# Kernel optimization log

Measured on AMD Instinct MI355X. Metric: run time of the kernel, lower is better.

## Reference

```python
import jax, jax.numpy as jnp
import numpy as np

B, C, H, W = 4, 128, 128, 128
K = 9          # 3x3 kernel taps
TAU, BETA = 0.5, 10.0


def conv3x3(x, w, b):
    # x: (B,Cin,H,W), w: (Cout,Cin,3,3), stride 1, padding 1
    y = jax.lax.conv_general_dilated(
        x, w, window_strides=(1, 1), padding=((1, 1), (1, 1)),
        dimension_numbers=('NCHW', 'OIHW', 'NCHW'))
    return y + b[None, :, None, None]


def bilinear_sample(x, py, px):
    # x: (B,C,H,W); py,px: (B,K,H,W) fractional coords -> (B,C,K,H,W), zero outside
    Hi, Wi = x.shape[2], x.shape[3]
    y0 = jnp.floor(py); x0 = jnp.floor(px)
    y1 = y0 + 1.0;      x1 = x0 + 1.0
    ly = py - y0; lx = px - x0
    hy = 1.0 - ly; hx = 1.0 - lx
    xf = x.reshape(x.shape[0], x.shape[1], -1)  # (B,C,HW)

    def corner(yc, xc, wgt):
        valid = (yc >= 0) & (yc <= Hi - 1) & (xc >= 0) & (xc <= Wi - 1)
        yi = jnp.clip(yc, 0, Hi - 1).astype(jnp.int32)
        xi = jnp.clip(xc, 0, Wi - 1).astype(jnp.int32)
        idx = (yi * Wi + xi).reshape(yc.shape[0], -1)  # (B, K*H*W)
        g = jax.vmap(lambda f, i: f[:, i])(xf, idx)    # (B,C,K*H*W)
        g = g.reshape(x.shape[0], x.shape[1], *yc.shape[1:])  # (B,C,K,H,W)
        return g * (wgt * valid.astype(wgt.dtype))[:, None]

    return (corner(y0, x0, hy * hx) + corner(y0, x1, hy * lx)
            + corner(y1, x0, ly * hx) + corner(y1, x1, ly * lx))


def modulated_dcn(x, offset, mask, w, b):
    # offset: (B,2K,H,W) layout (dy,dx) per tap; mask: (B,K,H,W)
    Bn, Cn, Hn, Wn = x.shape
    off = offset.reshape(Bn, K, 2, Hn, Wn)
    dy, dx = off[:, :, 0], off[:, :, 1]
    ky, kx = jnp.meshgrid(jnp.arange(3), jnp.arange(3), indexing='ij')
    base_y = (ky.reshape(-1) - 1).astype(x.dtype)  # dilation=1, padding=1, stride=1
    base_x = (kx.reshape(-1) - 1).astype(x.dtype)
    hh = jnp.arange(Hn, dtype=x.dtype)
    ww = jnp.arange(Wn, dtype=x.dtype)
    py = hh[None, None, :, None] + base_y[None, :, None, None] + dy  # (B,K,H,W)
    px = ww[None, None, None, :] + base_x[None, :, None, None] + dx
    samp = bilinear_sample(x, py, px) * mask[:, None]  # (B,C,K,H,W)
    out = jnp.einsum('bckhw,ock->bohw', samp, w.reshape(w.shape[0], w.shape[1], K))
    return out + b[None, :, None, None]


def setup_inputs() -> dict:
    key = jax.random.key(0)
    ks = jax.random.split(key, 8)
    x = jax.random.normal(ks[0], (B, C, H, W), dtype=jnp.float32)
    U = jax.random.uniform(ks[1], (B, 1, H, W), dtype=jnp.float32)
    # conv_offset_mask: (3*K, C+1, 3, 3); small scale -> offsets of O(1) pixel
    w_om = jax.random.normal(ks[2], (3 * K, C + 1, 3, 3), dtype=jnp.float32) * 0.01
    b_om = jnp.zeros((3 * K,), dtype=jnp.float32)
    kaiming = float(np.sqrt(2.0 / (C * 9)))
    w_dcn = jax.random.normal(ks[3], (C, C, 3, 3), dtype=jnp.float32) * kaiming
    b_dcn = jnp.zeros((C,), dtype=jnp.float32)
    w1 = jax.random.normal(ks[4], (C, C, 3, 3), dtype=jnp.float32) * kaiming
    b1 = jnp.zeros((C,), dtype=jnp.float32)
    w2 = jax.random.normal(ks[5], (C, C, 3, 3), dtype=jnp.float32) * float(np.sqrt(1.0 / (C * 9)))
    b2 = jnp.zeros((C,), dtype=jnp.float32)
    return {"x": x, "U": U, "w_om": w_om, "b_om": b_om, "w_dcn": w_dcn,
            "b_dcn": b_dcn, "w1": w1, "b1": b1, "w2": w2, "b2": b2}


def reference(x, U, w_om, b_om, w_dcn, b_dcn, w1, b1, w2, b2):
    U = jnp.clip(U, 0.0, 1.0)
    guide = jnp.concatenate([x, U], axis=1)                # (B,C+1,H,W)
    om = conv3x3(guide, w_om, b_om)                        # (B,3K,H,W)
    offset = om[:, :2 * K]
    mask = 2.0 * jax.nn.sigmoid(om[:, 2 * K:])
    z = modulated_dcn(x, offset, mask, w_dcn, b_dcn)
    r = jax.nn.relu(conv3x3(z, w1, b1))
    r = conv3x3(r, w2, b2)
    gate = jax.nn.sigmoid(BETA * (U - TAU))
    return jax.nn.relu(x + r * gate)
```

## Files before the change

kernel.cpp:

```cpp
#include <hip/hip_runtime.h>
#include <math.h>

typedef unsigned int uint;
typedef unsigned short ushort;
typedef __attribute__((ext_vector_type(8))) __bf16 bf16x8;
typedef __attribute__((ext_vector_type(2))) __bf16 bf16x2;
typedef __attribute__((ext_vector_type(4))) float f32x4;
typedef __attribute__((ext_vector_type(2))) float f32x2;

#define HW 16384

__device__ __forceinline__ ushort f2bf(float f) {
    uint u = __float_as_uint(f);
    u += 0x7fffu + ((u >> 16) & 1u);
    return (ushort)(u >> 16);
}
__device__ __forceinline__ void bhmap(int& b, int& h) {
    int lin = blockIdx.y * (int)gridDim.x + blockIdx.x;
    int n = (lin & 7) * 64 + (lin >> 3);
    h = n & 127;
    b = n >> 7;
}
__device__ __forceinline__ int swz(int row, int chunk) {
    return row * 128 + ((chunk ^ (row & 15)) << 3);
}
__device__ __forceinline__ void gl2lds16(const ushort* g, ushort* l) {
    __builtin_amdgcn_global_load_lds(
        (const __attribute__((address_space(1))) uint*)g,
        (__attribute__((address_space(3))) uint*)l,
        16, 0, 0);
}
__device__ __forceinline__ uint blend2(uint a, uint b, uint c, uint d,
                                       float w00, float w01, float w10, float w11) {
    f32x2 va = { __uint_as_float(a << 16), __uint_as_float(a & 0xffff0000u) };
    f32x2 vb = { __uint_as_float(b << 16), __uint_as_float(b & 0xffff0000u) };
    f32x2 vc = { __uint_as_float(c << 16), __uint_as_float(c & 0xffff0000u) };
    f32x2 vd = { __uint_as_float(d << 16), __uint_as_float(d & 0xffff0000u) };
    f32x2 v = va * w00 + vb * w01 + vc * w10 + vd * w11;
    bf16x2 pk; pk[0] = (__bf16)v[0]; pk[1] = (__bf16)v[1];
    uint r; __builtin_memcpy(&r, &pk, 4);
    return r;
}

__global__ __launch_bounds__(256) void prep_w(
    const float* __restrict__ wd, const float* __restrict__ w1,
    const float* __restrict__ w2, const float* __restrict__ wom,
    ushort* __restrict__ wdt, ushort* __restrict__ w1t,
    ushort* __restrict__ w2t, ushort* __restrict__ womt,
    float* __restrict__ womu)
{
    int i = blockIdx.x * 256 + threadIdx.x;
    if (i < 147456) {
        int k = i >> 14, oc = (i >> 7) & 127, d = i & 127;
        int ci = (((d >> 3) ^ (oc & 15)) << 3) | (d & 7);
        int s = (oc * 128 + ci) * 9 + k;
        wdt[i] = f2bf(wd[s]);
        w1t[i] = f2bf(w1[s]);
        w2t[i] = f2bf(w2[s]);
    }
    if (i < 36864) {
        int k = i >> 12, oc = (i >> 7) & 31, d = i & 127;
        int ci = (((d >> 3) ^ (oc & 15)) << 3) | (d & 7);
        womt[i] = (oc < 27) ? f2bf(wom[(oc * 129 + ci) * 9 + k]) : (ushort)0;
    }
    if (i < 288) {
        int k = i >> 5, oc = i & 31;
        womu[i] = (oc < 27) ? wom[(oc * 129 + 128) * 9 + k] : 0.f;
    }
}

__global__ __launch_bounds__(256) void prep_xt(
    const float* __restrict__ x, ushort* __restrict__ xt)
{
    int b, h; bhmap(b, h);
    const int tid = threadIdx.x;
    __shared__ __align__(16) ushort T[128 * 136];
    const int w0 = tid & 127, cg = tid >> 7;
#pragma unroll 4
    for (int it = 0; it < 64; it++) {
        int c = it * 2 + cg;
        float f = x[((size_t)(b * 128 + c)) * HW + h * 128 + w0];
        T[w0 * 136 + c] = f2bf(f);
    }
    __syncthreads();
    const int w1 = tid >> 1, half = tid & 1;
    uint4* dst = (uint4*)(xt + (((size_t)b * HW) + h * 128 + w1) * 128 + half * 64);
    const uint4* src = (const uint4*)&T[w1 * 136 + half * 64];
#pragma unroll
    for (int c8 = 0; c8 < 8; c8++) dst[c8] = src[c8];
}

__global__ __launch_bounds__(512, 4) void k_om(
    const ushort* __restrict__ xt, const float* __restrict__ U,
    const ushort* __restrict__ womt, const float* __restrict__ womu,
    const float* __restrict__ bom, float* __restrict__ omt)
{
    int b, h; bhmap(b, h);
    const int tid = threadIdx.x;
    const int wid = tid >> 6, lane = tid & 63, lq = lane & 15, quad = lane >> 4;
    const int pixbase = wid * 16;

    __shared__ __align__(16) ushort As[130 * 128];
    __shared__ __align__(16) ushort Bs[3][32 * 128];
    __shared__ float U3[3 * 130];
    __shared__ float wu[288];

    f32x4 acc[2];
#pragma unroll
    for (int j = 0; j < 2; j++)
#pragma unroll
        for (int r = 0; r < 4; r++) acc[j][r] = 0.f;

    for (int s = tid; s < 390; s += 512) {
        int r = s / 130, c = s % 130, gy = h - 1 + r, gx = c - 1;
        float v = 0.f;
        if ((unsigned)gy < 128u && (unsigned)gx < 128u) {
            v = U[(size_t)b * HW + gy * 128 + gx];
            v = fminf(fmaxf(v, 0.f), 1.f);
        }
        U3[s] = v;
    }
    if (tid < 288) wu[tid] = womu[tid];

    const size_t xb = (size_t)b * HW * 128;
#pragma unroll
    for (int dyi = 0; dyi < 3; dyi++) {
        int gy = h + dyi - 1;
        for (int c = tid; c < 2080; c += 512) {
            int r = c >> 4, ch = c & 15, gx = r - 1;
            uint4 v = {0, 0, 0, 0};
            if ((unsigned)gy < 128u && (unsigned)gx < 128u)
                v = *(const uint4*)(xt + xb + ((size_t)gy * 128 + gx) * 128 + ch * 8);
            *(uint4*)&As[swz(r, ch)] = v;
        }
#pragma unroll
        for (int t = 0; t < 3; t++)
            gl2lds16(womt + (dyi * 3 + t) * 4096 + tid * 8, &Bs[t][wid * 512]);
        __syncthreads();
#pragma unroll
        for (int dx = 0; dx < 3; dx++) {
#pragma unroll
            for (int kk = 0; kk < 4; kk++) {
                int chunk = kk * 4 + quad;
                bf16x8 av = *(const bf16x8*)&As[swz(pixbase + lq + dx, chunk)];
                bf16x8 bv[2];
#pragma unroll
                for (int j = 0; j < 2; j++) bv[j] = *(const bf16x8*)&Bs[dx][swz(j * 16 + lq, chunk)];
#pragma unroll
                for (int j = 0; j < 2; j++)
                    acc[j] = __builtin_amdgcn_mfma_f32_16x16x32_bf16(av, bv[j], acc[j], 0, 0, 0);
            }
        }
        __syncthreads();
    }

#pragma unroll
    for (int j = 0; j < 2; j++) {
        int oc = j * 16 + lq;
        if (oc < 27) {
            float bias = bom[oc];
#pragma unroll
            for (int r = 0; r < 4; r++) {
                int pix = pixbase + quad * 4 + r;
                float v = acc[j][r] + bias;
#pragma unroll
                for (int t = 0; t < 9; t++)
                    v += U3[(t / 3) * 130 + pix + (t % 3)] * wu[t * 32 + oc];
                if (oc >= 18) v = 2.f / (1.f + __expf(-v));
                omt[((size_t)b * HW + h * 128 + pix) * 32 + oc] = v;
            }
        }
    }
}

__global__ __launch_bounds__(512, 4) void k_dcn(
    const ushort* __restrict__ xt, const float* __restrict__ omt,
    const ushort* __restrict__ wdt, const float* __restrict__ bdcn,
    ushort* __restrict__ zt)
{
    int b, h; bhmap(b, h);
    const int tid = threadIdx.x;
    const int wid = tid >> 6, lane = tid & 63, lq = lane & 15, quad = lane >> 4;
    const int pixbase = (wid & 1) * 64, ocbase = (wid >> 1) * 32;

    __shared__ __align__(16) ushort As[128 * 128];
    __shared__ __align__(16) ushort Bs[128 * 128];
    __shared__ __align__(16) int tbl[2][128][8];

    const int sc = lane & 15;
    const int sp = lane >> 4;

    f32x4 acc[4][2];
#pragma unroll
    for (int i = 0; i < 4; i++)
#pragma unroll
        for (int j = 0; j < 2; j++)
#pragma unroll
            for (int r = 0; r < 4; r++) acc[i][j][r] = 0.f;

    const float* omrow = omt + ((size_t)b * HW + h * 128) * 32;
    const ushort* xtb = xt + (size_t)b * HW * 128;

    auto build = [&](int k, int buf) {
        if (tid < 128) {
            int p = tid;
            float dyv = omrow[p * 32 + 2 * k];
            float dxv = omrow[p * 32 + 2 * k + 1];
            float m   = omrow[p * 32 + 18 + k];
            float fy = (float)(h + k / 3 - 1) + dyv;
            float fx = (float)(p + k % 3 - 1) + dxv;
            float y0f = floorf(fy), x0f = floorf(fx);
            float ly = fy - y0f, lx = fx - x0f;
            float hy = 1.f - ly, hx = 1.f - lx;
            bool vy0 = (y0f >= 0.f) && (y0f <= 127.f);
            bool vy1 = (y0f >= -1.f) && (y0f <= 126.f);
            bool vx0 = (x0f >= 0.f) && (x0f <= 127.f);
            bool vx1 = (x0f >= -1.f) && (x0f <= 126.f);
            float w00 = (vy0 && vx0) ? hy * hx * m : 0.f;
            float w01 = (vy0 && vx1) ? hy * lx * m : 0.f;
            float w10 = (vy1 && vx0) ? ly * hx * m : 0.f;
            float w11 = (vy1 && vx1) ? ly * lx * m : 0.f;
            int iy0 = min(max((int)y0f, 0), 127);
            int iy1 = min(max((int)y0f + 1, 0), 127);
            int ix0 = min(max((int)x0f, 0), 127);
            int ix1 = min(max((int)x0f + 1, 0), 127);
            int* tp = &tbl[buf][p][0];
            tp[0] = (iy0 * 128 + ix0) * 128;
            tp[1] = (iy0 * 128 + ix1) * 128;
            tp[2] = (iy1 * 128 + ix0) * 128;
            tp[3] = (iy1 * 128 + ix1) * 128;
            ((float*)tp)[4] = w00; ((float*)tp)[5] = w01;
            ((float*)tp)[6] = w10; ((float*)tp)[7] = w11;
        }
    };

    build(0, 0);
    __syncthreads();

    for (int k = 0; k < 9; k++) {
        const int buf = k & 1;
        {
            const ushort* wsrc = wdt + (size_t)k * 16384;
#pragma unroll
            for (int c = 0; c < 4; c++)
                gl2lds16(wsrc + c * 4096 + tid * 8, &Bs[c * 4096 + wid * 512]);
        }
        const ushort* basep = xtb + sc * 8;
#pragma unroll 2
        for (int r = 0; r < 4; r++) {
            int p = r * 32 + wid * 4 + sp;
            int4 off = *(const int4*)&tbl[buf][p][0];
            f32x4 wv = *(const f32x4*)((const float*)&tbl[buf][p][0] + 4);
            uint4 q00 = *(const uint4*)(basep + off.x);
            uint4 q01 = *(const uint4*)(basep + off.y);
            uint4 q10 = *(const uint4*)(basep + off.z);
            uint4 q11 = *(const uint4*)(basep + off.w);
            uint4 st;
            st.x = blend2(q00.x, q01.x, q10.x, q11.x, wv[0], wv[1], wv[2], wv[3]);
            st.y = blend2(q00.y, q01.y, q10.y, q11.y, wv[0], wv[1], wv[2], wv[3]);
            st.z = blend2(q00.z, q01.z, q10.z, q11.z, wv[0], wv[1], wv[2], wv[3]);
            st.w = blend2(q00.w, q01.w, q10.w, q11.w, wv[0], wv[1], wv[2], wv[3]);
            *(uint4*)&As[swz(p, sc)] = st;
        }
        __syncthreads();
        if (k < 8) build(k + 1, buf ^ 1);
#pragma unroll
        for (int kk = 0; kk < 4; kk++) {
            int chunk = kk * 4 + quad;
            bf16x8 av[4], bv[2];
#pragma unroll
            for (int i = 0; i < 4; i++) av[i] = *(const bf16x8*)&As[swz(pixbase + i * 16 + lq, chunk)];
#pragma unroll
            for (int j = 0; j < 2; j++) bv[j] = *(const bf16x8*)&Bs[swz(ocbase + j * 16 + lq, chunk)];
#pragma unroll
            for (int i = 0; i < 4; i++)
#pragma unroll
                for (int j = 0; j < 2; j++)
                    acc[i][j] = __builtin_amdgcn_mfma_f32_16x16x32_bf16(av[i], bv[j], acc[i][j], 0, 0, 0);
        }
        __syncthreads();
    }

    size_t prow = ((size_t)b * HW + h * 128) * 128;
#pragma unroll
    for (int j = 0; j < 2; j++) {
        int oc = ocbase + j * 16 + lq;
        float bias = bdcn[oc];
#pragma unroll
        for (int i = 0; i < 4; i++)
#pragma unroll
            for (int r = 0; r < 4; r++) {
                int pix = pixbase + i * 16 + quad * 4 + r;
                zt[prow + (size_t)pix * 128 + oc] = f2bf(acc[i][j][r] + bias);
            }
    }
}

__global__ __launch_bounds__(512, 4) void k_conv1(
    const ushort* __restrict__ zt, const ushort* __restrict__ w1t,
    const float* __restrict__ b1, ushort* __restrict__ r1t)
{
    int b, h; bhmap(b, h);
    const int tid = threadIdx.x;
    const int wid = tid >> 6, lane = tid & 63, lq = lane & 15, quad = lane >> 4;
    const int pixbase = (wid & 1) * 64, ocbase = (wid >> 1) * 32;

    __shared__ __align__(16) ushort As[130 * 128];
    __shared__ __align__(16) ushort Bs[128 * 128];

    f32x4 acc[4][2];
#pragma unroll
    for (int i = 0; i < 4; i++)
#pragma unroll
        for (int j = 0; j < 2; j++)
#pragma unroll
            for (int r = 0; r < 4; r++) acc[i][j][r] = 0.f;

    const size_t zb = (size_t)b * HW * 128;
    for (int t9 = 0; t9 < 9; t9++) {
        const int dyi = t9 / 3, dx = t9 % 3;
        if (dx == 0) {
            int gy = h + dyi - 1;
            for (int c = tid; c < 2080; c += 512) {
                int r = c >> 4, ch = c & 15, gx = r - 1;
                uint4 v = {0, 0, 0, 0};
                if ((unsigned)gy < 128u && (unsigned)gx < 128u)
                    v = *(const uint4*)(zt + zb + ((size_t)gy * 128 + gx) * 128 + ch * 8);
                *(uint4*)&As[swz(r, ch)] = v;
            }
        }
        {
            const ushort* wsrc = w1t + (size_t)t9 * 16384;
#pragma unroll
            for (int c = 0; c < 4; c++)
                gl2lds16(wsrc + c * 4096 + tid * 8, &Bs[c * 4096 + wid * 512]);
        }
        __syncthreads();
#pragma unroll
        for (int kk = 0; kk < 4; kk++) {
            int chunk = kk * 4 + quad;
            bf16x8 av[4], bv[2];
#pragma unroll
            for (int i = 0; i < 4; i++)
                av[i] = *(const bf16x8*)&As[swz(pixbase + i * 16 + lq + dx, chunk)];
#pragma unroll
            for (int j = 0; j < 2; j++) bv[j] = *(const bf16x8*)&Bs[swz(ocbase + j * 16 + lq, chunk)];
#pragma unroll
            for (int i = 0; i < 4; i++)
#pragma unroll
                for (int j = 0; j < 2; j++)
                    acc[i][j] = __builtin_amdgcn_mfma_f32_16x16x32_bf16(av[i], bv[j], acc[i][j], 0, 0, 0);
        }
        __syncthreads();
    }

    size_t prow = ((size_t)b * HW + h * 128) * 128;
#pragma unroll
    for (int j = 0; j < 2; j++) {
        int oc = ocbase + j * 16 + lq;
        float bias = b1[oc];
#pragma unroll
        for (int i = 0; i < 4; i++)
#pragma unroll
            for (int r = 0; r < 4; r++) {
                int pix = pixbase + i * 16 + quad * 4 + r;
                r1t[prow + (size_t)pix * 128 + oc] = f2bf(fmaxf(acc[i][j][r] + bias, 0.f));
            }
    }
}

__global__ __launch_bounds__(512, 4) void k_conv2(
    const ushort* __restrict__ r1t, const ushort* __restrict__ w2t,
    const float* __restrict__ b2, const float* __restrict__ x,
    const float* __restrict__ U, float* __restrict__ out)
{
    int b, h; bhmap(b, h);
    const int tid = threadIdx.x;
    const int wid = tid >> 6, lane = tid & 63, lq = lane & 15, quad = lane >> 4;
    const int mbase = (wid & 1) * 64;
    const int nbase = (wid >> 1) * 32;

    __shared__ __align__(16) ushort As[128 * 128];
    __shared__ __align__(16) ushort Bs[130 * 128];

    f32x4 acc[4][2];
#pragma unroll
    for (int i = 0; i < 4; i++)
#pragma unroll
        for (int j = 0; j < 2; j++)
#pragma unroll
            for (int r = 0; r < 4; r++) acc[i][j][r] = 0.f;

    const size_t rb = (size_t)b * HW * 128;
    for (int t9 = 0; t9 < 9; t9++) {
        const int dyi = t9 / 3, dx = t9 % 3;
        if (dx == 0) {
            int gy = h + dyi - 1;
            for (int c = tid; c < 2080; c += 512) {
                int r = c >> 4, ch = c & 15, gx = r - 1;
                uint4 v = {0, 0, 0, 0};
                if ((unsigned)gy < 128u && (unsigned)gx < 128u)
                    v = *(const uint4*)(r1t + rb + ((size_t)gy * 128 + gx) * 128 + ch * 8);
                *(uint4*)&Bs[swz(r, ch)] = v;
            }
        }
        {
            const ushort* wsrc = w2t + (size_t)t9 * 16384;
#pragma unroll
            for (int c = 0; c < 4; c++)
                gl2lds16(wsrc + c * 4096 + tid * 8, &As[c * 4096 + wid * 512]);
        }
        __syncthreads();
#pragma unroll
        for (int kk = 0; kk < 4; kk++) {
            int chunk = kk * 4 + quad;
            bf16x8 av[4], bv[2];
#pragma unroll
            for (int i = 0; i < 4; i++) av[i] = *(const bf16x8*)&As[swz(mbase + i * 16 + lq, chunk)];
#pragma unroll
            for (int j = 0; j < 2; j++)
                bv[j] = *(const bf16x8*)&Bs[swz(nbase + j * 16 + lq + dx, chunk)];
#pragma unroll
            for (int i = 0; i < 4; i++)
#pragma unroll
                for (int j = 0; j < 2; j++)
                    acc[i][j] = __builtin_amdgcn_mfma_f32_16x16x32_bf16(av[i], bv[j], acc[i][j], 0, 0, 0);
        }
        __syncthreads();
    }

#pragma unroll
    for (int j = 0; j < 2; j++) {
        int pix = nbase + j * 16 + lq;
        float u = U[(size_t)b * HW + h * 128 + pix];
        u = fminf(fmaxf(u, 0.f), 1.f);
        float g = 1.f / (1.f + __expf(-10.f * (u - 0.5f)));
#pragma unroll
        for (int i = 0; i < 4; i++) {
            f32x4 b4 = *(const f32x4*)&b2[mbase + i * 16 + quad * 4];
#pragma unroll
            for (int r = 0; r < 4; r++) {
                int oc = mbase + i * 16 + quad * 4 + r;
                size_t idx = ((size_t)(b * 128 + oc)) * HW + h * 128 + pix;
                float v = acc[i][j][r] + b4[r];
                out[idx] = fmaxf(x[idx] + v * g, 0.f);
            }
        }
    }
}

extern "C" void kernel_launch(void* const* d_in, const int* in_sizes, int n_in,
                              void* d_out, int out_size, void* d_ws, size_t ws_size,
                              hipStream_t stream)
{
    const float* x     = (const float*)d_in[0];
    const float* U     = (const float*)d_in[1];
    const float* w_om  = (const float*)d_in[2];
    const float* b_om  = (const float*)d_in[3];
    const float* w_dcn = (const float*)d_in[4];
    const float* b_dcn = (const float*)d_in[5];
    const float* w1    = (const float*)d_in[6];
    const float* b1    = (const float*)d_in[7];
    const float* w2    = (const float*)d_in[8];
    const float* b2    = (const float*)d_in[9];
    float* out = (float*)d_out;

    char* p = (char*)d_ws;
    ushort* xt   = (ushort*)p; p += (size_t)4 * HW * 128 * 2;
    ushort* zt   = (ushort*)p; p += (size_t)4 * HW * 128 * 2;
    ushort* r1t  = (ushort*)p; p += (size_t)4 * HW * 128 * 2;
    float*  omt  = (float*)p;  p += (size_t)4 * HW * 32 * 4;
    ushort* wdt  = (ushort*)p; p += 147456 * 2;
    ushort* w1t  = (ushort*)p; p += 147456 * 2;
    ushort* w2t  = (ushort*)p; p += 147456 * 2;
    ushort* womt = (ushort*)p; p += 36864 * 2;
    float*  womu = (float*)p;  p += 288 * 4;

    prep_w<<<576, 256, 0, stream>>>(w_dcn, w1, w2, w_om, wdt, w1t, w2t, womt, womu);
    prep_xt<<<dim3(128, 4), 256, 0, stream>>>(x, xt);
    k_om<<<dim3(128, 4), 512, 0, stream>>>(xt, U, womt, womu, b_om, omt);
    k_dcn<<<dim3(128, 4), 512, 0, stream>>>(xt, omt, wdt, b_dcn, zt);
    k_conv1<<<dim3(128, 4), 512, 0, stream>>>(zt, w1t, b1, r1t);
    k_conv2<<<dim3(128, 4), 512, 0, stream>>>(r1t, w2t, b2, x, U, out);
}
```

Baseline: 216.0 us.

## Process two output rows per block in conv1/conv2 to share weight tiles

Each conv block now covers two image rows with 1024 threads instead of one row with 512, so every per-tap 128x128 weight tile loaded into LDS feeds twice as many MFMAs. This halves weight traffic from global memory and the LDS fill work per output row. The cost is a larger LDS footprint (about 98 KB for the two input-row tiles plus the weight tile) and half as many blocks (256), which limits occupancy and how many blocks run concurrently per CU.

```diff
diff --git a/kernel.cpp b/kernel.cpp
--- a/kernel.cpp
+++ b/kernel.cpp
@@ -20,6 +20,12 @@
     int n = (lin & 7) * 64 + (lin >> 3);
     h = n & 127;
     b = n >> 7;
+}
+__device__ __forceinline__ void bhmap2r(int& b, int& h0) {
+    int lin = blockIdx.y * (int)gridDim.x + blockIdx.x;
+    int n = (lin & 7) * 32 + (lin >> 3);
+    h0 = (n & 63) * 2;
+    b = n >> 6;
 }
 __device__ __forceinline__ int swz(int row, int chunk) {
     return row * 128 + ((chunk ^ (row & 15)) << 3);
@@ -296,16 +302,19 @@
     }
 }
 
-__global__ __launch_bounds__(512, 4) void k_conv1(
+__global__ __launch_bounds__(1024, 4) void k_conv1(
     const ushort* __restrict__ zt, const ushort* __restrict__ w1t,
     const float* __restrict__ b1, ushort* __restrict__ r1t)
 {
-    int b, h; bhmap(b, h);
+    int b, h0; bhmap2r(b, h0);
     const int tid = threadIdx.x;
     const int wid = tid >> 6, lane = tid & 63, lq = lane & 15, quad = lane >> 4;
-    const int pixbase = (wid & 1) * 64, ocbase = (wid >> 1) * 32;
-
-    __shared__ __align__(16) ushort As[130 * 128];
+    const int row = wid >> 3;
+    const int pixbase = (wid & 1) * 64;
+    const int ocbase = ((wid >> 1) & 3) * 32;
+    const int rowoff = row * 16640;
+
+    __shared__ __align__(16) ushort As[2 * 130 * 128];
     __shared__ __align__(16) ushort Bs[128 * 128];
 
     f32x4 acc[4][2];
@@ -320,20 +329,23 @@
     for (int t9 = 0; t9 < 9; t9++) {
         const int dyi = t9 / 3, dx = t9 % 3;
         if (dx == 0) {
-            int gy = h + dyi - 1;
-            for (int c = tid; c < 2080; c += 512) {
-                int r = c >> 4, ch = c & 15, gx = r - 1;
-                uint4 v = {0, 0, 0, 0};
-                if ((unsigned)gy < 128u && (unsigned)gx < 128u)
-                    v = *(const uint4*)(zt + zb + ((size_t)gy * 128 + gx) * 128 + ch * 8);
-                *(uint4*)&As[swz(r, ch)] = v;
+#pragma unroll
+            for (int rr = 0; rr < 2; rr++) {
+                int gy = h0 + rr + dyi - 1;
+                for (int c = tid; c < 2080; c += 1024) {
+                    int r = c >> 4, ch = c & 15, gx = r - 1;
+                    uint4 v = {0, 0, 0, 0};
+                    if ((unsigned)gy < 128u && (unsigned)gx < 128u)
+                        v = *(const uint4*)(zt + zb + ((size_t)gy * 128 + gx) * 128 + ch * 8);
+                    *(uint4*)&As[rr * 16640 + swz(r, ch)] = v;
+                }
             }
         }
         {
             const ushort* wsrc = w1t + (size_t)t9 * 16384;
 #pragma unroll
-            for (int c = 0; c < 4; c++)
-                gl2lds16(wsrc + c * 4096 + tid * 8, &Bs[c * 4096 + wid * 512]);
+            for (int c = 0; c < 2; c++)
+                gl2lds16(wsrc + c * 8192 + tid * 8, &Bs[c * 8192 + wid * 512]);
         }
         __syncthreads();
 #pragma unroll
@@ -342,7 +354,7 @@
             bf16x8 av[4], bv[2];
 #pragma unroll
             for (int i = 0; i < 4; i++)
-                av[i] = *(const bf16x8*)&As[swz(pixbase + i * 16 + lq + dx, chunk)];
+                av[i] = *(const bf16x8*)&As[rowoff + swz(pixbase + i * 16 + lq + dx, chunk)];
 #pragma unroll
             for (int j = 0; j < 2; j++) bv[j] = *(const bf16x8*)&Bs[swz(ocbase + j * 16 + lq, chunk)];
 #pragma unroll
@@ -354,7 +366,7 @@
         __syncthreads();
     }
 
-    size_t prow = ((size_t)b * HW + h * 128) * 128;
+    size_t prow = ((size_t)b * HW + (h0 + row) * 128) * 128;
 #pragma unroll
     for (int j = 0; j < 2; j++) {
         int oc = ocbase + j * 16 + lq;
@@ -369,19 +381,21 @@
     }
 }
 
-__global__ __launch_bounds__(512, 4) void k_conv2(
+__global__ __launch_bounds__(1024, 4) void k_conv2(
     const ushort* __restrict__ r1t, const ushort* __restrict__ w2t,
     const float* __restrict__ b2, const float* __restrict__ x,
     const float* __restrict__ U, float* __restrict__ out)
 {
-    int b, h; bhmap(b, h);
+    int b, h0; bhmap2r(b, h0);
     const int tid = threadIdx.x;
     const int wid = tid >> 6, lane = tid & 63, lq = lane & 15, quad = lane >> 4;
+    const int row = wid >> 3;
     const int mbase = (wid & 1) * 64;
-    const int nbase = (wid >> 1) * 32;
+    const int nbase = ((wid >> 1) & 3) * 32;
+    const int rowoff = row * 16640;
 
     __shared__ __align__(16) ushort As[128 * 128];
-    __shared__ __align__(16) ushort Bs[130 * 128];
+    __shared__ __align__(16) ushort Bs[2 * 130 * 128];
 
     f32x4 acc[4][2];
 #pragma unroll
@@ -395,20 +409,23 @@
     for (int t9 = 0; t9 < 9; t9++) {
         const int dyi = t9 / 3, dx = t9 % 3;
         if (dx == 0) {
-            int gy = h + dyi - 1;
-            for (int c = tid; c < 2080; c += 512) {
-                int r = c >> 4, ch = c & 15, gx = r - 1;
-                uint4 v = {0, 0, 0, 0};
-                if ((unsigned)gy < 128u && (unsigned)gx < 128u)
-                    v = *(const uint4*)(r1t + rb + ((size_t)gy * 128 + gx) * 128 + ch * 8);
-                *(uint4*)&Bs[swz(r, ch)] = v;
+#pragma unroll
+            for (int rr = 0; rr < 2; rr++) {
+                int gy = h0 + rr + dyi - 1;
+                for (int c = tid; c < 2080; c += 1024) {
+                    int r = c >> 4, ch = c & 15, gx = r - 1;
+                    uint4 v = {0, 0, 0, 0};
+                    if ((unsigned)gy < 128u && (unsigned)gx < 128u)
+                        v = *(const uint4*)(r1t + rb + ((size_t)gy * 128 + gx) * 128 + ch * 8);
+                    *(uint4*)&Bs[rr * 16640 + swz(r, ch)] = v;
+                }
             }
         }
         {
             const ushort* wsrc = w2t + (size_t)t9 * 16384;
 #pragma unroll
-            for (int c = 0; c < 4; c++)
-                gl2lds16(wsrc + c * 4096 + tid * 8, &As[c * 4096 + wid * 512]);
+            for (int c = 0; c < 2; c++)
+                gl2lds16(wsrc + c * 8192 + tid * 8, &As[c * 8192 + wid * 512]);
         }
         __syncthreads();
 #pragma unroll
@@ -419,7 +436,7 @@
             for (int i = 0; i < 4; i++) av[i] = *(const bf16x8*)&As[swz(mbase + i * 16 + lq, chunk)];
 #pragma unroll
             for (int j = 0; j < 2; j++)
-                bv[j] = *(const bf16x8*)&Bs[swz(nbase + j * 16 + lq + dx, chunk)];
+                bv[j] = *(const bf16x8*)&Bs[rowoff + swz(nbase + j * 16 + lq + dx, chunk)];
 #pragma unroll
             for (int i = 0; i < 4; i++)
 #pragma unroll
@@ -429,6 +446,7 @@
         __syncthreads();
     }
 
+    const int h = h0 + row;
 #pragma unroll
     for (int j = 0; j < 2; j++) {
         int pix = nbase + j * 16 + lq;
@@ -480,6 +498,6 @@
     prep_xt<<<dim3(128, 4), 256, 0, stream>>>(x, xt);
     k_om<<<dim3(128, 4), 512, 0, stream>>>(xt, U, womt, womu, b_om, omt);
     k_dcn<<<dim3(128, 4), 512, 0, stream>>>(xt, omt, wdt, b_dcn, zt);
-    k_conv1<<<dim3(128, 4), 512, 0, stream>>>(zt, w1t, b1, r1t);
-    k_conv2<<<dim3(128, 4), 512, 0, stream>>>(r1t, w2t, b2, x, U, out);
-}
+    k_conv1<<<dim3(64, 4), 1024, 0, stream>>>(zt, w1t, b1, r1t);
+    k_conv2<<<dim3(64, 4), 1024, 0, stream>>>(r1t, w2t, b2, x, U, out);
+}
```

Result: no change. 215.9 us (-0.0%).
